# Optimization experiments

Measured on AMD Instinct MI355X. Metric: run time of the kernel, lower is better.

Reference implementation:

```python
import jax, jax.numpy as jnp
import numpy as np

NEG_INF = jnp.float32(-2**32 + 1)  # matches the module's padding constant


def setup_inputs() -> dict:
    key = jax.random.key(0)
    ks = jax.random.split(key, 20)
    T, N, E, R = 4, 20000, 320000, 2
    Din, Dh, H = 64, 64, 4
    s = 0.1  # xavier-ish scale
    inp = {
        "x": jax.random.normal(ks[0], (T, N, Din), jnp.float32),
        "edge_index": jax.random.randint(ks[1], (T, R, 2, E), 0, N, jnp.int32),
        "W_src": jax.random.normal(ks[2], (R, Din, H * Dh), jnp.float32) * s,
        "W_dst": jax.random.normal(ks[3], (R, Din, H * Dh), jnp.float32) * s,
        "att_src": jax.random.normal(ks[4], (R, H, Dh), jnp.float32) * s,
        "att_dst": jax.random.normal(ks[5], (R, H, Dh), jnp.float32) * s,
        "ra_W1": jax.random.normal(ks[6], (Dh, 4 * Dh), jnp.float32) * s,
        "ra_b1": jnp.zeros((4 * Dh,), jnp.float32),
        "ra_W2": jax.random.normal(ks[7], (4 * Dh, 1), jnp.float32) * s,
        "lstm_Wih": jax.random.normal(ks[8], (4 * Dh, Dh), jnp.float32) * s,
        "lstm_Whh": jax.random.normal(ks[9], (4 * Dh, Dh), jnp.float32) * s,
        "lstm_bih": jnp.zeros((4 * Dh,), jnp.float32),
        "lstm_bhh": jnp.zeros((4 * Dh,), jnp.float32),
        "pos_emb": jax.random.normal(ks[10], (T, Dh), jnp.float32) * s,
        "Wq": jax.random.normal(ks[11], (Dh, Dh), jnp.float32) * s,
        "Wk": jax.random.normal(ks[12], (Dh, Dh), jnp.float32) * s,
        "Wv": jax.random.normal(ks[13], (Dh, Dh), jnp.float32) * s,
    }
    return inp


def _gat(xt, ei, Ws, Wd, a_s, a_d, N, H, C):
    # PyG GATConv, concat=False, bias=False, eval mode (no dropout)
    src, dst = ei[0], ei[1]
    hs = (xt @ Ws).reshape(N, H, C)
    hd = (xt @ Wd).reshape(N, H, C)
    als = (hs * a_s[None]).sum(-1)          # [N,H]
    ald = (hd * a_d[None]).sum(-1)          # [N,H]
    e = jax.nn.leaky_relu(als[src] + ald[dst], 0.2)   # [E,H]
    m = jax.ops.segment_max(e, dst, num_segments=N)   # [N,H]
    p = jnp.exp(e - m[dst])
    denom = jax.ops.segment_sum(p, dst, num_segments=N)
    alpha = p / (denom[dst] + 1e-16)
    out = jax.ops.segment_sum(hs[src] * alpha[:, :, None], dst, num_segments=N)  # [N,H,C]
    return out.mean(1)                      # concat=False -> mean over heads


def reference(x, edge_index, W_src, W_dst, att_src, att_dst,
              ra_W1, ra_b1, ra_W2,
              lstm_Wih, lstm_Whh, lstm_bih, lstm_bhh,
              pos_emb, Wq, Wk, Wv):
    T, N, _ = x.shape
    R, H, C = att_src.shape   # C == n_hid (per-head GAT channels)

    # ---- intra-relation aggregation: GATConv per etype, vmapped over timeframes
    intra = []
    for r in range(R):
        f = jax.vmap(lambda xt, ei, r=r: _gat(xt, ei, W_src[r], W_dst[r],
                                              att_src[r], att_dst[r], N, H, C))
        intra.append(f(x, edge_index[:, r]))      # [T,N,C]
    h = jnp.stack(intra, axis=2)                  # [T,N,R,C]

    # ---- inter-relation aggregation (RelationAgg), batched over timeframes
    s = jnp.tanh(h @ ra_W1 + ra_b1) @ ra_W2       # [T,N,R,1]
    beta = jax.nn.softmax(s.mean(1), axis=1)      # mean over nodes, softmax over R -> [T,R,1]
    inter = (beta[:, None] * h).sum(2)            # [T,N,C]

    # ---- LSTM over time (batch = nodes)
    def step(carry, xt):
        hh, cc = carry
        g = xt @ lstm_Wih.T + hh @ lstm_Whh.T + lstm_bih + lstm_bhh
        i, f_, gg, o = jnp.split(g, 4, axis=-1)   # torch gate order i,f,g,o
        cc = jax.nn.sigmoid(f_) * cc + jax.nn.sigmoid(i) * jnp.tanh(gg)
        hh = jax.nn.sigmoid(o) * jnp.tanh(cc)
        return (hh, cc), hh
    z = jnp.zeros((N, C), x.dtype)
    _, hs_seq = jax.lax.scan(step, (z, z), inter)  # [T,N,C]
    feats = hs_seq.transpose(1, 0, 2)              # [N,T,C]

    # ---- temporal multi-head attention with causal mask, eval mode
    Ch = C // H
    ti = feats + pos_emb[None]                     # positions are just arange(T)
    qh = (ti @ Wq).reshape(N, T, H, Ch)
    kh = (ti @ Wk).reshape(N, T, H, Ch)
    vh = (ti @ Wv).reshape(N, T, H, Ch)
    scores = jnp.einsum('nqhc,nkhc->nhqk', qh, kh) / jnp.sqrt(jnp.float32(T))
    mask = jnp.tril(jnp.ones((T, T), bool))
    scores = jnp.where(mask[None, None], scores, NEG_INF)
    a = jax.nn.softmax(scores, axis=-1)
    out = jnp.einsum('nhqk,nkhc->nqhc', a, vh).reshape(N, T, C)
    return out  # output_features[ttype][ntype] == out[:, i, :]
```

## Files before the change

kernel.cpp:

```cpp
#include <hip/hip_runtime.h>
#include <hip/hip_bf16.h>

#define T_ 4
#define N_ 20000
#define E_ 320000
#define R_ 2
#define DIN 64
#define G_ 256
#define P_ 8
#define BPAD 16384
#define NB_ 32
#define EPB_ 10000
#define CHN_ 625

typedef unsigned short u16;
typedef __attribute__((ext_vector_type(8))) short bf16x8;
typedef __attribute__((ext_vector_type(2))) _Float16 h2;
typedef __attribute__((ext_vector_type(4))) float f32x4;

__device__ __forceinline__ float bf2f(u16 u) {
    unsigned int i = ((unsigned int)u) << 16; float f;
    __builtin_memcpy(&f, &i, 4); return f;
}
__device__ __forceinline__ u16 f2bf(float f) {
    unsigned int i; __builtin_memcpy(&i, &f, 4);
    unsigned int r = i + 0x7fffu + ((i >> 16) & 1u);
    return (u16)(r >> 16);
}
__device__ __forceinline__ u16 f2h(float f) {
    union { _Float16 h; u16 u; } c; c.h = (_Float16)f; return c.u;
}
__device__ __forceinline__ float sigm(float x) { return 1.f / (1.f + __expf(-x)); }
__device__ __forceinline__ float ftanh(float x) { return 1.f - 2.f / (__expf(2.f * x) + 1.f); }
__device__ __forceinline__ float rdlanef(float v, int l) {
    int i; __builtin_memcpy(&i, &v, 4);
    int r = __builtin_amdgcn_readlane(i, l);
    float f; __builtin_memcpy(&f, &r, 4); return f;
}
__device__ __forceinline__ float fdot2(h2 a, h2 b, float c) {
#if __has_builtin(__builtin_amdgcn_fdot2)
    return __builtin_amdgcn_fdot2(a, b, c, false);
#else
    float r;
    asm("v_dot2_f32_f16 %0, %1, %2, %3" : "=v"(r) : "v"(a), "v"(b), "v"(c));
    return r;
#endif
}
__device__ __forceinline__ unsigned cvtpk_bf16(float lo, float hi) {
    unsigned r;
    asm("v_cvt_pk_bf16_f32 %0, %1, %2" : "=v"(r) : "v"(lo), "v"(hi));
    return r;
}

__device__ __forceinline__ void gemm_direct(
    const u16* __restrict__ A, const u16* __restrict__ Bpad,
    int M, int Astride, int kchunks, int m0, f32x4* acc)
{
    const int tid = threadIdx.x;
    const int lane = tid & 63, wv = tid >> 6;
    const int col = lane & 15, quad = lane >> 4;
    #pragma unroll
    for (int cf = 0; cf < 16; ++cf) { acc[cf][0]=0.f; acc[cf][1]=0.f; acc[cf][2]=0.f; acc[cf][3]=0.f; }

    int row = m0 + wv * 16 + col;
    int row_c = (row < M) ? row : (M - 1);

    for (int kc = 0; kc < kchunks; ++kc) {
        #pragma unroll
        for (int ks = 0; ks < 2; ++ks) {
            bf16x8 a = *(const bf16x8*)(A + (size_t)row_c * Astride + kc * 64 + ks * 32 + quad * 8);
            const u16* bb = Bpad + kc * BPAD + ks * 32 + quad * 8;
            #pragma unroll
            for (int cf = 0; cf < 16; ++cf) {
                bf16x8 b = *(const bf16x8*)(bb + (cf * 16 + col) * 64);
                acc[cf] = __builtin_amdgcn_mfma_f32_16x16x32_bf16(a, b, acc[cf], 0, 0, 0);
            }
        }
    }
}

__global__ __launch_bounds__(256) void k_fold(
    const float* __restrict__ x, const float* __restrict__ wdall,
    float* __restrict__ als_all, float* __restrict__ ald_all, u16* __restrict__ x_h)
{
    __shared__ float wds[1024];
    {
        int tid = threadIdx.x;
        *(float4*)(wds + tid * 4) = *(const float4*)(wdall + tid * 4);
    }
    __syncthreads();

    int t = blockIdx.y;
    int idx = blockIdx.x * 256 + threadIdx.x;
    if (idx >= N_ * 4) return;
    int n = idx >> 2, q = idx & 3;
    const float* xr = x + ((size_t)t * N_ + n) * 64 + q * 16;
    float4 xv[4];
    #pragma unroll
    for (int i = 0; i < 4; ++i) xv[i] = *(const float4*)(xr + i * 4);

    {
        union { u16 h[16]; ushort4 s4[4]; } cv;
        #pragma unroll
        for (int i = 0; i < 4; ++i) {
            cv.h[i*4+0] = f2h(xv[i].x); cv.h[i*4+1] = f2h(xv[i].y);
            cv.h[i*4+2] = f2h(xv[i].z); cv.h[i*4+3] = f2h(xv[i].w);
        }
        u16* xo = x_h + ((size_t)t * N_ + n) * 64 + q * 16;
        #pragma unroll
        for (int i = 0; i < 4; ++i) *(ushort4*)(xo + i * 4) = cv.s4[i];
    }

    float s[16];
    #pragma unroll
    for (int i = 0; i < 16; ++i) s[i] = 0.f;
    #pragma unroll
    for (int i = 0; i < 4; ++i) {
        float xe[4] = {xv[i].x, xv[i].y, xv[i].z, xv[i].w};
        #pragma unroll
        for (int e = 0; e < 4; ++e) {
            int k = q * 16 + i * 4 + e;
            float xk = xe[e];
            #pragma unroll
            for (int tb = 0; tb < 4; ++tb) {
                float4 w = *(const float4*)(wds + tb * 256 + k * 4);
                s[tb*4+0] += xk * w.x; s[tb*4+1] += xk * w.y;
                s[tb*4+2] += xk * w.z; s[tb*4+3] += xk * w.w;
            }
        }
    }
    #pragma unroll
    for (int i = 0; i < 16; ++i) {
        s[i] += __shfl_xor(s[i], 1);
        s[i] += __shfl_xor(s[i], 2);
    }
    if (q == 0) {
        *(float4*)(als_all + ((size_t)(t*2+0) * N_ + n) * 4) = make_float4(s[0], s[1], s[2], s[3]);
        *(float4*)(als_all + ((size_t)(t*2+1) * N_ + n) * 4) = make_float4(s[4], s[5], s[6], s[7]);
        *(float4*)(ald_all + ((size_t)(t*2+0) * N_ + n) * 4) = make_float4(s[8], s[9], s[10], s[11]);
        *(float4*)(ald_all + ((size_t)(t*2+1) * N_ + n) * 4) = make_float4(s[12], s[13], s[14], s[15]);
    }
}

__global__ void k_prep(const float* __restrict__ Wdst, const float* __restrict__ att_dst,
                       const float* __restrict__ Wih, const float* __restrict__ Whh,
                       const float* __restrict__ bih, const float* __restrict__ bhh,
                       const float* __restrict__ Wsrc, const float* __restrict__ att_src,
                       const float* __restrict__ raW1,
                       const float* __restrict__ Wq, const float* __restrict__ Wk,
                       const float* __restrict__ Wv,
                       float* __restrict__ wdall, float* __restrict__ biasv,
                       u16* __restrict__ raW1_pad, u16* __restrict__ Wc_pad,
                       u16* __restrict__ qkv_pad, u16* __restrict__ postB_pad,
                       float* __restrict__ sspart)
{
    int tid = threadIdx.x, bid = blockIdx.x;
    if (bid == 0) {
        for (int i = tid; i < 1024; i += 256) sspart[i] = 0.f;
        int k = tid >> 2, h = tid & 3;
        for (int r = 0; r < 2; ++r) {
            float ss = 0.f, sd = 0.f;
            for (int c = 0; c < 64; ++c) {
                ss += Wsrc[((size_t)r * 64 + k) * 256 + h * 64 + c] * att_src[r * 256 + h * 64 + c];
                sd += Wdst[((size_t)r * 64 + k) * 256 + h * 64 + c] * att_dst[r * 256 + h * 64 + c];
            }
            wdall[r * 256 + k * 4 + h] = ss;
            wdall[512 + r * 256 + k * 4 + h] = sd;
        }
        biasv[tid] = bih[tid] + bhh[tid];
    }
    for (int i = bid * 256 + tid; i < BPAD; i += gridDim.x * 256) {
        int n = i >> 6, kk = i & 63;
        raW1_pad[i] = f2bf(raW1[kk * 256 + n]);
    }
    for (int i = bid * 256 + tid; i < 2 * BPAD; i += gridDim.x * 256) {
        int kc = i >> 14, q = i & (BPAD - 1), n = q >> 6, kk = q & 63;
        const float* W = kc ? Whh : Wih;
        Wc_pad[i] = f2bf(W[n * 64 + kk]);
    }
    for (int i = bid * 256 + tid; i < 192 * 64; i += gridDim.x * 256) {
        int g = i >> 6, kk = i & 63;
        int j = g >> 6, c = g & 63;
        const float* W = (j == 0) ? Wq : (j == 1) ? Wk : Wv;
        qkv_pad[i] = f2bf(W[kk * 64 + c]);
    }
    for (int i = bid * 256 + tid; i < 2 * 4 * 4096; i += gridDim.x * 256) {
        int r = i >> 14, q = i & 16383, kc = q >> 12, qq = q & 4095;
        int c = qq >> 6, kk = qq & 63;
        int d = kc * 16 + (kk >> 2), h = kk & 3;
        postB_pad[i] = f2bf(Wsrc[(size_t)r * 16384 + d * 256 + h * 64 + c]);
    }
}

__global__ __launch_bounds__(256) void k_hist(const int* __restrict__ ei,
                                              u16* __restrict__ rank, u16* __restrict__ partial)
{
    __shared__ unsigned int hist[N_ / 2];
    int b = blockIdx.x, p = blockIdx.y, tid = threadIdx.x;
    for (int i = tid; i < N_ / 2; i += 256) hist[i] = 0u;
    __syncthreads();
    const int* dsts = ei + ((size_t)p * 2 + 1) * E_ + b * EPB_;
    u16* rk = rank + (size_t)p * E_ + b * EPB_;
    for (int e = tid; e < EPB_; e += 256) {
        int dst = dsts[e];
        unsigned sh = (unsigned)(dst & 1) * 16u;
        unsigned old = atomicAdd(&hist[dst >> 1], 1u << sh);
        rk[e] = (u16)((old >> sh) & 0xffffu);
    }
    __syncthreads();
    u16* part = partial + ((size_t)p * NB_ + b) * N_;
    for (int n = tid; n < N_; n += 256) {
        unsigned hv = hist[n >> 1];
        part[n] = (u16)((hv >> ((unsigned)(n & 1) * 16u)) & 0xffffu);
    }
}

__global__ __launch_bounds__(256) void k_scan1(u16* __restrict__ partial,
                                               int* __restrict__ offsets, int* __restrict__ chunktot)
{
    int p = blockIdx.y, ch = blockIdx.x;
    int tid = threadIdx.x, lane = tid & 63, wid = tid >> 6;
    __shared__ int wtot[4];
    u16* part = partial + (size_t)p * NB_ * N_;
    int* ofs = offsets + (size_t)p * (N_ + 1);
    int n0 = ch * CHN_;
    int carry = 0;
    for (int rnd = 0; rnd < 3; ++rnd) {
        int i = rnd * 256 + tid;
        int n = n0 + i;
        int v = 0;
        if (i < CHN_) {
            int run = 0;
            #pragma unroll 8
            for (int b = 0; b < NB_; ++b) {
                int pv = part[b * N_ + n];
                part[b * N_ + n] = (u16)run;
                run += pv;
            }
            v = run;
        }
        int incl = v;
        for (int d = 1; d < 64; d <<= 1) { int u = __shfl_up(incl, d); if (lane >= d) incl += u; }
        if (lane == 63) wtot[wid] = incl;
        __syncthreads();
        if (tid < 4) {
            int iv = wtot[tid];
            for (int d = 1; d < 4; d <<= 1) { int u = __shfl_up(iv, d); if (tid >= d) iv += u; }
            wtot[tid] = iv;
        }
        __syncthreads();
        int woff = (wid > 0) ? wtot[wid - 1] : 0;
        int tot = wtot[3];
        int excl = carry + woff + incl - v;
        if (i < CHN_) ofs[n] = excl;
        carry += tot;
        __syncthreads();
    }
    if (tid == 0) chunktot[p * NB_ + ch] = carry;
}

__global__ void k_scan3(int* __restrict__ offsets, const int* __restrict__ chunktot) {
    __shared__ int cb[NB_];
    int p = blockIdx.y;
    int tid = threadIdx.x;
    if (tid < 64) {
        int v = (tid < NB_) ? chunktot[p * NB_ + tid] : 0;
        #pragma unroll
        for (int d = 1; d < NB_; d <<= 1) { int u = __shfl_up(v, d); if (tid >= d) v += u; }
        if (tid < NB_) cb[tid] = v;
    }
    __syncthreads();
    int n = blockIdx.x * 256 + tid;
    if (n < N_) {
        int c = n / CHN_;
        int base = (c > 0) ? cb[c - 1] : 0;
        offsets[(size_t)p * (N_ + 1) + n] += base;
    }
    if (n == 0)
        offsets[(size_t)p * (N_ + 1) + N_] = E_;
}

__global__ void k_scatter(const int* __restrict__ ei, const int* __restrict__ offsets,
                          const u16* __restrict__ rank, const u16* __restrict__ partial,
                          u16* __restrict__ csr) {
    int bid = blockIdx.x;
    int p = bid & 7;
    int e = (bid >> 3) * 256 + threadIdx.x;
    int src = ei[((size_t)p * 2 + 0) * E_ + e];
    int dst = ei[((size_t)p * 2 + 1) * E_ + e];
    int b = e / EPB_;
    int pos = offsets[p * (N_ + 1) + dst]
            + (int)partial[((size_t)p * NB_ + b) * N_ + dst]
            + (int)rank[(size_t)p * E_ + e];
    csr[(size_t)p * E_ + pos] = (u16)src;
}

__global__ __launch_bounds__(256) void k_agg(
    const int* __restrict__ offsets, const u16* __restrict__ csr,
    const float* __restrict__ als_all, const float* __restrict__ ald_all,
    const u16* __restrict__ x_h, u16* __restrict__ xagg4)
{
    __shared__ __align__(16) u16 ptab[4][4][64];
    const int bid = blockIdx.x;
    const int p = bid & 7;
    const int t = p >> 1;
    const int* off   = offsets + (size_t)p * (N_ + 1);
    const u16* srcs  = csr + (size_t)p * E_;
    const float* als = als_all + (size_t)p * N_ * 4;
    const float* ald = ald_all + (size_t)p * N_ * 4;
    const u16* xb    = x_h + (size_t)t * N_ * 64;

    const int tid = threadIdx.x, lane = tid & 63, wv = tid >> 6;
    const int g = lane >> 4, el = lane & 15;
    const int n0 = (bid >> 3) * 16 + wv * 4;
    const int ng = n0 + g;
    const int o0 = off[ng], o1 = off[ng + 1];
    const int deg = o1 - o0;
    const float4 aldv = *(const float4*)(ald + (size_t)ng * 4);
    u16* pt = &ptab[wv][0][0];
    const int pw = g * 64 + (el >> 1) * 8 + (el & 1);

    int sdeg[4];
    #pragma unroll
    for (int q = 0; q < 4; ++q) sdeg[q] = __builtin_amdgcn_readlane(deg, q * 16);
    int mdeg = max(max(sdeg[0], sdeg[1]), max(sdeg[2], sdeg[3]));
    int nrounds = (mdeg + 15) >> 4;

    float acc[4][4];
    #pragma unroll
    for (int q = 0; q < 4; ++q)
        #pragma unroll
        for (int h = 0; h < 4; ++h) acc[q][h] = 0.f;
    float d0 = 0.f, d1 = 0.f, d2 = 0.f, d3 = 0.f;

    for (int rr = 0; rr < nrounds; ++rr) {
        int e = rr * 16 + el;
        int sv = 0;
        float p0 = 0.f, p1 = 0.f, p2 = 0.f, p3 = 0.f;
        if (e < deg) {
            sv = (int)srcs[o0 + e];
            float4 av = *(const float4*)(als + (size_t)sv * 4);
            float e0 = av.x + aldv.x, e1 = av.y + aldv.y;
            float e2 = av.z + aldv.z, e3 = av.w + aldv.w;
            e0 = fmaxf(e0, 0.2f * e0); e1 = fmaxf(e1, 0.2f * e1);
            e2 = fmaxf(e2, 0.2f * e2); e3 = fmaxf(e3, 0.2f * e3);
            p0 = __expf(e0); p1 = __expf(e1); p2 = __expf(e2); p3 = __expf(e3);
        }
        d0 += p0; d1 += p1; d2 += p2; d3 += p3;
        pt[pw + 0] = f2h(p0); pt[pw + 2] = f2h(p1);
        pt[pw + 4] = f2h(p2); pt[pw + 6] = f2h(p3);
        #pragma unroll
        for (int q = 0; q < 4; ++q) {
            int rem = sdeg[q] - rr * 16;
            if (rem > 0) {
                const u16* ptq = pt + q * 64;
                unsigned xl0[8], xl1[8];
                #pragma unroll
                for (int pr = 0; pr < 8; ++pr) {
                    if (pr * 2 < rem) {
                        int s0i = __builtin_amdgcn_readlane(sv, q * 16 + pr * 2);
                        int s1i = __builtin_amdgcn_readlane(sv, q * 16 + pr * 2 + 1);
                        xl0[pr] = xb[((size_t)(unsigned)s0i << 6) + lane];
                        xl1[pr] = xb[((size_t)(unsigned)s1i << 6) + lane];
                    }
                }
                #pragma unroll
                for (int pr = 0; pr < 8; ++pr) {
                    if (pr * 2 < rem) {
                        unsigned xp = xl0[pr] | (xl1[pr] << 16);
                        uint4 ppv = *(const uint4*)(ptq + pr * 8);
                        h2 xv, q0, q1, q2, q3;
                        __builtin_memcpy(&xv, &xp, 4);
                        __builtin_memcpy(&q0, &ppv.x, 4);
                        __builtin_memcpy(&q1, &ppv.y, 4);
                        __builtin_memcpy(&q2, &ppv.z, 4);
                        __builtin_memcpy(&q3, &ppv.w, 4);
                        acc[q][0] = fdot2(xv, q0, acc[q][0]);
                        acc[q][1] = fdot2(xv, q1, acc[q][1]);
                        acc[q][2] = fdot2(xv, q2, acc[q][2]);
                        acc[q][3] = fdot2(xv, q3, acc[q][3]);
                    }
                }
            }
        }
    }
    d0 += __shfl_xor(d0, 1); d0 += __shfl_xor(d0, 2);
    d0 += __shfl_xor(d0, 4); d0 += __shfl_xor(d0, 8);
    d1 += __shfl_xor(d1, 1); d1 += __shfl_xor(d1, 2);
    d1 += __shfl_xor(d1, 4); d1 += __shfl_xor(d1, 8);
    d2 += __shfl_xor(d2, 1); d2 += __shfl_xor(d2, 2);
    d2 += __shfl_xor(d2, 4); d2 += __shfl_xor(d2, 8);
    d3 += __shfl_xor(d3, 1); d3 += __shfl_xor(d3, 2);
    d3 += __shfl_xor(d3, 4); d3 += __shfl_xor(d3, 8);
    float inv0 = 0.25f / (d0 + 1e-16f);
    float inv1 = 0.25f / (d1 + 1e-16f);
    float inv2 = 0.25f / (d2 + 1e-16f);
    float inv3 = 0.25f / (d3 + 1e-16f);
    #pragma unroll
    for (int q = 0; q < 4; ++q) {
        float s0 = rdlanef(inv0, q * 16);
        float s1 = rdlanef(inv1, q * 16);
        float s2 = rdlanef(inv2, q * 16);
        float s3 = rdlanef(inv3, q * 16);
        unsigned w01 = cvtpk_bf16(acc[q][0] * s0, acc[q][1] * s1);
        unsigned w23 = cvtpk_bf16(acc[q][2] * s2, acc[q][3] * s3);
        *(uint2*)(xagg4 + ((size_t)p * N_ + n0 + q) * 256 + lane * 4) = make_uint2(w01, w23);
    }
}

__global__ __launch_bounds__(256) void k_post(
    const u16* __restrict__ xagg4, const u16* __restrict__ postB_pad,
    u16* __restrict__ intra)
{
    const int t = blockIdx.z, r = blockIdx.y;
    const u16* A = xagg4 + ((size_t)(t * 2 + r)) * N_ * 256;
    const u16* Bp = postB_pad + (size_t)r * 4 * 4096;
    const int tid = threadIdx.x, lane = tid & 63, wv = tid >> 6;
    const int col = lane & 15, quad = lane >> 4;
    int m0 = blockIdx.x * 64;
    int row = m0 + wv * 16 + col;
    int row_c = (row < N_) ? row : (N_ - 1);

    f32x4 acc[4];
    #pragma unroll
    for (int cf = 0; cf < 4; ++cf) { acc[cf][0]=0.f; acc[cf][1]=0.f; acc[cf][2]=0.f; acc[cf][3]=0.f; }
    #pragma unroll
    for (int kc = 0; kc < 4; ++kc) {
        #pragma unroll
        for (int ks = 0; ks < 2; ++ks) {
            bf16x8 a = *(const bf16x8*)(A + (size_t)row_c * 256 + kc * 64 + ks * 32 + quad * 8);
            const u16* bb = Bp + kc * 4096 + ks * 32 + quad * 8;
            #pragma unroll
            for (int cf = 0; cf < 4; ++cf) {
                bf16x8 b = *(const bf16x8*)(bb + (cf * 16 + col) * 64);
                acc[cf] = __builtin_amdgcn_mfma_f32_16x16x32_bf16(a, b, acc[cf], 0, 0, 0);
            }
        }
    }
    int rowbase = m0 + wv * 16 + quad * 4;
    #pragma unroll
    for (int cf = 0; cf < 4; ++cf) {
        int c = cf * 16 + col;
        #pragma unroll
        for (int reg = 0; reg < 4; ++reg) {
            int rr = rowbase + reg;
            if (rr < N_)
                intra[(((size_t)t * N_ + rr) * 2 + r) * 64 + c] = f2bf(acc[cf][reg]);
        }
    }
}

__global__ __launch_bounds__(256) void k_relagg(
    const u16* __restrict__ A, const u16* __restrict__ W1pad, const float* __restrict__ b1,
    const float* __restrict__ W2, float* __restrict__ sspart)
{
    int m0 = blockIdx.x * 64;
    f32x4 acc[16];
    gemm_direct(A, W1pad, T_ * N_ * R_, 64, 1, m0, acc);

    const int tid = threadIdx.x, lane = tid & 63, wv = tid >> 6;
    const int col = lane & 15;
    float sp[4] = {0.f, 0.f, 0.f, 0.f};
    #pragma unroll
    for (int cf = 0; cf < 16; ++cf) {
        int gcol = cf * 16 + col;
        float bb = b1[gcol];
        float ww = W2[gcol];
        #pragma unroll
        for (int reg = 0; reg < 4; ++reg)
            sp[reg] += ftanh(acc[cf][reg] + bb) * ww;
    }
    #pragma unroll
    for (int reg = 0; reg < 4; ++reg) {
        float v = sp[reg];
        v += __shfl_xor(v, 1); v += __shfl_xor(v, 2);
        v += __shfl_xor(v, 4); v += __shfl_xor(v, 8);
        sp[reg] = v;
    }
    float se = sp[0] + sp[2];
    float so = sp[1] + sp[3];
    se += __shfl_xor(se, 16); se += __shfl_xor(se, 32);
    so += __shfl_xor(so, 16); so += __shfl_xor(so, 32);
    __shared__ float red[8];
    if (lane == 0) { red[wv * 2] = se; red[wv * 2 + 1] = so; }
    __syncthreads();
    if (tid == 0) {
        float s0 = red[0] + red[2] + red[4] + red[6];
        float s1 = red[1] + red[3] + red[5] + red[7];
        int t = m0 / (N_ * R_);
        float* line = sspart + (blockIdx.x & 63) * 16;
        atomicAdd(&line[t * 2 + 0], s0);
        atomicAdd(&line[t * 2 + 1], s1);
    }
}

__global__ __launch_bounds__(256) void k_lstm(
    const u16* __restrict__ intra, const float* __restrict__ sspart,
    const u16* __restrict__ Wc_pad, const float* __restrict__ biasv,
    u16* __restrict__ feats)
{
    __shared__ __align__(16) u16 wtab[512][64];
    __shared__ __align__(16) u16 hl[64][72];
    __shared__ float betas_s[8];
    const int tid = threadIdx.x, lane = tid & 63, wv = tid >> 6;
    const int col = lane & 15, quad = lane >> 4;
    int m0 = blockIdx.x * 64;
    int row = m0 + wv * 16 + col;
    int row_c = (row < N_) ? row : (N_ - 1);
    int rowbase = m0 + wv * 16 + quad * 4;

    bf16x8 pi[4][4];
    #pragma unroll
    for (int t = 0; t < 4; ++t) {
        const u16* ib = intra + ((size_t)t * N_ + row_c) * 128;
        #pragma unroll
        for (int k = 0; k < 4; ++k)
            pi[t][k] = *(const bf16x8*)(ib + k * 32 + quad * 8);
    }

    {
        const uint4* src = (const uint4*)Wc_pad;
        #pragma unroll
        for (int it = 0; it < 16; ++it) {
            int u = it * 256 + tid;
            int r = u >> 3, s = u & 7;
            uint4 v = src[u];
            *(uint4*)((char*)&wtab[0][0] + (size_t)r * 128 + ((s ^ (r & 7)) * 16)) = v;
        }
    }
    if (tid < 64) {
        float a8[8];
        #pragma unroll
        for (int s = 0; s < 8; ++s) a8[s] = sspart[tid * 16 + s];
        #pragma unroll
        for (int s = 0; s < 8; ++s) {
            float v = a8[s];
            v += __shfl_xor(v, 1); v += __shfl_xor(v, 2);
            v += __shfl_xor(v, 4); v += __shfl_xor(v, 8);
            v += __shfl_xor(v, 16); v += __shfl_xor(v, 32);
            a8[s] = v;
        }
        if (tid < 4) {
            float s0 = a8[tid * 2] * (1.f / N_), s1 = a8[tid * 2 + 1] * (1.f / N_);
            float mx = fmaxf(s0, s1);
            float e0 = __expf(s0 - mx), e1 = __expf(s1 - mx);
            float inv = 1.f / (e0 + e1);
            betas_s[tid * 2] = e0 * inv; betas_s[tid * 2 + 1] = e1 * inv;
        }
    }
    __syncthreads();
    float betas[8];
    #pragma unroll
    for (int i = 0; i < 8; ++i) betas[i] = betas_s[i];

    float cc[4][4];
    #pragma unroll
    for (int j = 0; j < 4; ++j)
        #pragma unroll
        for (int reg = 0; reg < 4; ++reg) cc[j][reg] = 0.f;

    const int c7 = col & 7;
    #pragma unroll
    for (int t = 0; t < 4; ++t) {
        float b0 = betas[t * 2], b1 = betas[t * 2 + 1];

        f32x4 acc[16];
        #pragma unroll
        for (int cf = 0; cf < 16; ++cf) { acc[cf][0]=0.f; acc[cf][1]=0.f; acc[cf][2]=0.f; acc[cf][3]=0.f; }

        #pragma unroll
        for (int ks = 0; ks < 2; ++ks) {
            bf16x8 i0 = pi[t][ks];
            bf16x8 i1 = pi[t][2 + ks];
            union { u16 h[8]; bf16x8 v; } cv;
            #pragma unroll
            for (int j = 0; j < 8; ++j)
                cv.h[j] = f2bf(b0 * bf2f((u16)i0[j]) + b1 * bf2f((u16)i1[j]));
            #pragma unroll
            for (int cf = 0; cf < 16; ++cf) {
                bf16x8 b = *(const bf16x8*)((const char*)&wtab[0][0]
                    + (size_t)(cf * 16 + col) * 128 + (((ks * 4 + quad) ^ c7) * 16));
                acc[cf] = __builtin_amdgcn_mfma_f32_16x16x32_bf16(cv.v, b, acc[cf], 0, 0, 0);
            }
        }
        if (t > 0) {
            #pragma unroll
            for (int ks = 0; ks < 2; ++ks) {
                bf16x8 a = *(const bf16x8*)&hl[wv * 16 + col][ks * 32 + quad * 8];
                #pragma unroll
                for (int cf = 0; cf < 16; ++cf) {
                    bf16x8 b = *(const bf16x8*)((const char*)&wtab[0][0]
                        + (size_t)(256 + cf * 16 + col) * 128 + (((ks * 4 + quad) ^ c7) * 16));
                    acc[cf] = __builtin_amdgcn_mfma_f32_16x16x32_bf16(a, b, acc[cf], 0, 0, 0);
                }
            }
        }

        #pragma unroll
        for (int j = 0; j < 4; ++j) {
            int c = j * 16 + col;
            float bi = biasv[c], bf_ = biasv[64 + c], bg = biasv[128 + c], bo = biasv[192 + c];
            #pragma unroll
            for (int reg = 0; reg < 4; ++reg) {
                float gi = acc[j][reg] + bi;
                float gf = acc[j + 4][reg] + bf_;
                float gg = acc[j + 8][reg] + bg;
                float go = acc[j + 12][reg] + bo;
                float c2 = sigm(gf) * cc[j][reg] + sigm(gi) * ftanh(gg);
                float hh = sigm(go) * ftanh(c2);
                cc[j][reg] = c2;
                u16 hb = f2bf(hh);
                hl[wv * 16 + quad * 4 + reg][c] = hb;
                int rr = rowbase + reg;
                if (rr < N_)
                    feats[(size_t)rr * 256 + t * 64 + c] = hb;
            }
        }
    }
}

__global__ __launch_bounds__(256) void k_attn(
    const u16* __restrict__ feats, const float* __restrict__ pos_emb,
    const u16* __restrict__ qkv_pad, float* __restrict__ out)
{
    __shared__ float qkv_s[64 * 200];
    const int tid = threadIdx.x, lane = tid & 63, wv = tid >> 6;
    const int col = lane & 15, quad = lane >> 4;
    int m0 = blockIdx.x * 64;
    int row = m0 + wv * 16 + col;
    int trow = row & 3;

    f32x4 acc[12];
    #pragma unroll
    for (int cf = 0; cf < 12; ++cf) { acc[cf][0]=0.f; acc[cf][1]=0.f; acc[cf][2]=0.f; acc[cf][3]=0.f; }
    #pragma unroll
    for (int ks = 0; ks < 2; ++ks) {
        int coff = ks * 32 + quad * 8;
        bf16x8 fv = *(const bf16x8*)(feats + (size_t)row * 64 + coff);
        float4 p0 = *(const float4*)(pos_emb + trow * 64 + coff);
        float4 p1 = *(const float4*)(pos_emb + trow * 64 + coff + 4);
        union { u16 h[8]; bf16x8 v; } cv;
        cv.h[0] = f2bf(bf2f((u16)fv[0]) + p0.x); cv.h[1] = f2bf(bf2f((u16)fv[1]) + p0.y);
        cv.h[2] = f2bf(bf2f((u16)fv[2]) + p0.z); cv.h[3] = f2bf(bf2f((u16)fv[3]) + p0.w);
        cv.h[4] = f2bf(bf2f((u16)fv[4]) + p1.x); cv.h[5] = f2bf(bf2f((u16)fv[5]) + p1.y);
        cv.h[6] = f2bf(bf2f((u16)fv[6]) + p1.z); cv.h[7] = f2bf(bf2f((u16)fv[7]) + p1.w);
        bf16x8 a = cv.v;
        const u16* bb = qkv_pad + ks * 32 + quad * 8;
        #pragma unroll
        for (int cf = 0; cf < 12; ++cf) {
            bf16x8 b = *(const bf16x8*)(bb + (cf * 16 + col) * 64);
            acc[cf] = __builtin_amdgcn_mfma_f32_16x16x32_bf16(a, b, acc[cf], 0, 0, 0);
        }
    }
    #pragma unroll
    for (int cf = 0; cf < 12; ++cf) {
        int g = cf * 16 + col;
        #pragma unroll
        for (int reg = 0; reg < 4; ++reg) {
            int rl = wv * 16 + quad * 4 + reg;
            qkv_s[rl * 200 + g] = acc[cf][reg];
        }
    }
    __syncthreads();

    int nl = wv * 4 + (lane >> 4);
    int sub = lane & 15;
    int h = sub >> 2, tq = sub & 3;
    const float* qrow = qkv_s + (nl * 4 + tq) * 200 + h * 16;

    float s[4];
    #pragma unroll
    for (int tk = 0; tk < 4; ++tk) {
        const float* krow = qkv_s + (nl * 4 + tk) * 200 + 64 + h * 16;
        float d = 0.f;
        #pragma unroll
        for (int j = 0; j < 16; ++j) d += qrow[j] * krow[j];
        s[tk] = (tk > tq) ? -4294967295.0f : d * 0.5f;
    }
    float mx = fmaxf(fmaxf(s[0], s[1]), fmaxf(s[2], s[3]));
    float a0 = __expf(s[0]-mx), a1 = __expf(s[1]-mx), a2 = __expf(s[2]-mx), a3 = __expf(s[3]-mx);
    float inv = 1.f / (a0 + a1 + a2 + a3);
    a0 *= inv; a1 *= inv; a2 *= inv; a3 *= inv;

    int n = blockIdx.x * 16 + nl;
    const float* v0 = qkv_s + (nl * 4 + 0) * 200 + 128 + h * 16;
    const float* v1 = v0 + 200, *v2 = v0 + 400, *v3 = v0 + 600;
    #pragma unroll
    for (int cc4 = 0; cc4 < 4; ++cc4) {
        float4 o;
        o.x = a0*v0[cc4*4+0] + a1*v1[cc4*4+0] + a2*v2[cc4*4+0] + a3*v3[cc4*4+0];
        o.y = a0*v0[cc4*4+1] + a1*v1[cc4*4+1] + a2*v2[cc4*4+1] + a3*v3[cc4*4+1];
        o.z = a0*v0[cc4*4+2] + a1*v1[cc4*4+2] + a2*v2[cc4*4+2] + a3*v3[cc4*4+2];
        o.w = a0*v0[cc4*4+3] + a1*v1[cc4*4+3] + a2*v2[cc4*4+3] + a3*v3[cc4*4+3];
        *(float4*)(out + (size_t)n * 256 + tq * 64 + h * 16 + cc4 * 4) = o;
    }
}

extern "C" void kernel_launch(void* const* d_in, const int* in_sizes, int n_in,
                              void* d_out, int out_size, void* d_ws, size_t ws_size,
                              hipStream_t stream) {
    const float* x     = (const float*)d_in[0];
    const int* ei      = (const int*)d_in[1];
    const float* Wsrc  = (const float*)d_in[2];
    const float* Wdst  = (const float*)d_in[3];
    const float* att_src = (const float*)d_in[4];
    const float* att_dst = (const float*)d_in[5];
    const float* raW1  = (const float*)d_in[6];
    const float* rab1  = (const float*)d_in[7];
    const float* raW2  = (const float*)d_in[8];
    const float* Wih   = (const float*)d_in[9];
    const float* Whh   = (const float*)d_in[10];
    const float* bih   = (const float*)d_in[11];
    const float* bhh   = (const float*)d_in[12];
    const float* pos   = (const float*)d_in[13];
    const float* Wq    = (const float*)d_in[14];
    const float* Wk    = (const float*)d_in[15];
    const float* Wv    = (const float*)d_in[16];
    float* out = (float*)d_out;

    char* w = (char*)d_ws;
    size_t off = 0;
    auto alloc = [&](size_t bytes) -> char* {
        char* pp = w + off; off += (bytes + 255) & ~(size_t)255; return pp;
    };
    u16*   intra     = (u16*)  alloc((size_t)T_ * N_ * R_ * 64 * 2);
    u16*   x_h       = (u16*)  alloc((size_t)T_ * N_ * 64 * 2);
    float* sspart    = (float*)alloc(1024 * 4);
    float* wdall     = (float*)alloc(1024 * 4);
    float* biasv     = (float*)alloc(256 * 4);
    u16*   raW1_pad  = (u16*)  alloc(BPAD * 2);
    u16*   Wc_pad    = (u16*)  alloc(2 * BPAD * 2);
    u16*   qkv_pad   = (u16*)  alloc(192 * 64 * 2);
    u16*   postB_pad = (u16*)  alloc(2 * 4 * 4096 * 2);
    int*   chunktot  = (int*)  alloc(P_ * NB_ * 4);
    char*  ubase   = alloc(0);
    size_t uoff = 0;
    auto ualloc = [&](size_t bytes) -> char* {
        char* pp = ubase + uoff; uoff += (bytes + 255) & ~(size_t)255; return pp;
    };
    int*   offsets = (int*)  ualloc((size_t)P_ * (N_ + 1) * 4);
    u16*   csr     = (u16*)  ualloc((size_t)P_ * E_ * 2);
    float* als_all = (float*)ualloc((size_t)P_ * N_ * 4 * 4);
    float* ald_all = (float*)ualloc((size_t)P_ * N_ * 4 * 4);
    u16*   partial = (u16*)  ualloc((size_t)P_ * NB_ * N_ * 2);
    u16*   xagg4   = (u16*)  ualloc((size_t)P_ * N_ * 256 * 2);
    u16*   rank    = (u16*)  xagg4;
    u16*   feats   = (u16*)  ubase;
    (void)ws_size; (void)in_sizes; (void)n_in; (void)out_size;

    k_prep<<<72, 256, 0, stream>>>(Wdst, att_dst, Wih, Whh, bih, bhh, Wsrc, att_src, raW1,
                                   Wq, Wk, Wv, wdall, biasv, raW1_pad, Wc_pad, qkv_pad,
                                   postB_pad, sspart);
    k_hist<<<dim3(NB_, 8), 256, 0, stream>>>(ei, rank, partial);
    k_scan1<<<dim3(NB_, 8), 256, 0, stream>>>(partial, offsets, chunktot);
    k_scan3<<<dim3(79, 8), 256, 0, stream>>>(offsets, chunktot);
    k_scatter<<<10000, 256, 0, stream>>>(ei, offsets, rank, partial, csr);
    k_fold<<<dim3(313, 4), 256, 0, stream>>>(x, wdall, als_all, ald_all, x_h);
    k_agg<<<10000, 256, 0, stream>>>(offsets, csr, als_all, ald_all, x_h, xagg4);
    k_post<<<dim3(313, 2, 4), 256, 0, stream>>>(xagg4, postB_pad, intra);
    k_relagg<<<2500, 256, 0, stream>>>(intra, raW1_pad, rab1, raW2, sspart);
    k_lstm<<<313, 256, 0, stream>>>(intra, sspart, Wc_pad, biasv, feats);
    k_attn<<<1250, 256, 0, stream>>>(feats, pos, qkv_pad, out);
}
```

Baseline: 419.6 us.

## Fuse post-aggregation projection GEMM into k_agg via swizzled shared tile

The separate k_post kernel is removed. k_agg now stages its 16x256 bf16 per-head aggregates in an XOR-swizzled shared buffer and runs the projection with MFMA directly, writing intra. This avoids a 41 MB xagg4 round trip through global memory and one kernel launch. A second change adds a fast path for full 16-edge rounds that skips the per-pair bound checks. The cost is extra LDS, a __syncthreads, and a small MFMA tail in every block.

After: 397.9 us. 1.05x faster.

```diff
diff --git a/kernel.cpp b/kernel.cpp
--- a/kernel.cpp
+++ b/kernel.cpp
@@ -298,12 +298,14 @@
 __global__ __launch_bounds__(256) void k_agg(
     const int* __restrict__ offsets, const u16* __restrict__ csr,
     const float* __restrict__ als_all, const float* __restrict__ ald_all,
-    const u16* __restrict__ x_h, u16* __restrict__ xagg4)
+    const u16* __restrict__ x_h, const u16* __restrict__ postB_pad,
+    u16* __restrict__ intra)
 {
     __shared__ __align__(16) u16 ptab[4][4][64];
+    __shared__ __align__(16) u16 xs[16 * 256];
     const int bid = blockIdx.x;
     const int p = bid & 7;
-    const int t = p >> 1;
+    const int t = p >> 1, rel = p & 1;
     const int* off   = offsets + (size_t)p * (N_ + 1);
     const u16* srcs  = csr + (size_t)p * E_;
     const float* als = als_all + (size_t)p * N_ * 4;
@@ -312,7 +314,8 @@
 
     const int tid = threadIdx.x, lane = tid & 63, wv = tid >> 6;
     const int g = lane >> 4, el = lane & 15;
-    const int n0 = (bid >> 3) * 16 + wv * 4;
+    const int nb0 = (bid >> 3) * 16;
+    const int n0 = nb0 + wv * 4;
     const int ng = n0 + g;
     const int o0 = off[ng], o1 = off[ng + 1];
     const int deg = o1 - o0;
@@ -352,7 +355,32 @@
         #pragma unroll
         for (int q = 0; q < 4; ++q) {
             int rem = sdeg[q] - rr * 16;
-            if (rem > 0) {
+            if (rem >= 16) {
+                const u16* ptq = pt + q * 64;
+                unsigned xl0[8], xl1[8];
+                #pragma unroll
+                for (int pr = 0; pr < 8; ++pr) {
+                    int s0i = __builtin_amdgcn_readlane(sv, q * 16 + pr * 2);
+                    int s1i = __builtin_amdgcn_readlane(sv, q * 16 + pr * 2 + 1);
+                    xl0[pr] = xb[((size_t)(unsigned)s0i << 6) + lane];
+                    xl1[pr] = xb[((size_t)(unsigned)s1i << 6) + lane];
+                }
+                #pragma unroll
+                for (int pr = 0; pr < 8; ++pr) {
+                    unsigned xp = xl0[pr] | (xl1[pr] << 16);
+                    uint4 ppv = *(const uint4*)(ptq + pr * 8);
+                    h2 xv, q0, q1, q2, q3;
+                    __builtin_memcpy(&xv, &xp, 4);
+                    __builtin_memcpy(&q0, &ppv.x, 4);
+                    __builtin_memcpy(&q1, &ppv.y, 4);
+                    __builtin_memcpy(&q2, &ppv.z, 4);
+                    __builtin_memcpy(&q3, &ppv.w, 4);
+                    acc[q][0] = fdot2(xv, q0, acc[q][0]);
+                    acc[q][1] = fdot2(xv, q1, acc[q][1]);
+                    acc[q][2] = fdot2(xv, q2, acc[q][2]);
+                    acc[q][3] = fdot2(xv, q3, acc[q][3]);
+                }
+            } else if (rem > 0) {
                 const u16* ptq = pt + q * 64;
                 unsigned xl0[8], xl1[8];
                 #pragma unroll
@@ -404,48 +432,31 @@
         float s3 = rdlanef(inv3, q * 16);
         unsigned w01 = cvtpk_bf16(acc[q][0] * s0, acc[q][1] * s1);
         unsigned w23 = cvtpk_bf16(acc[q][2] * s2, acc[q][3] * s3);
-        *(uint2*)(xagg4 + ((size_t)p * N_ + n0 + q) * 256 + lane * 4) = make_uint2(w01, w23);
-    }
-}
-
-__global__ __launch_bounds__(256) void k_post(
-    const u16* __restrict__ xagg4, const u16* __restrict__ postB_pad,
-    u16* __restrict__ intra)
-{
-    const int t = blockIdx.z, r = blockIdx.y;
-    const u16* A = xagg4 + ((size_t)(t * 2 + r)) * N_ * 256;
-    const u16* Bp = postB_pad + (size_t)r * 4 * 4096;
-    const int tid = threadIdx.x, lane = tid & 63, wv = tid >> 6;
-    const int col = lane & 15, quad = lane >> 4;
-    int m0 = blockIdx.x * 64;
-    int row = m0 + wv * 16 + col;
-    int row_c = (row < N_) ? row : (N_ - 1);
-
-    f32x4 acc[4];
-    #pragma unroll
-    for (int cf = 0; cf < 4; ++cf) { acc[cf][0]=0.f; acc[cf][1]=0.f; acc[cf][2]=0.f; acc[cf][3]=0.f; }
-    #pragma unroll
-    for (int kc = 0; kc < 4; ++kc) {
-        #pragma unroll
-        for (int ks = 0; ks < 2; ++ks) {
-            bf16x8 a = *(const bf16x8*)(A + (size_t)row_c * 256 + kc * 64 + ks * 32 + quad * 8);
-            const u16* bb = Bp + kc * 4096 + ks * 32 + quad * 8;
+        int rowt = wv * 4 + q;
+        char* dst = (char*)xs + rowt * 512 + (((lane >> 1) ^ (rowt & 7)) * 16) + (lane & 1) * 8;
+        *(uint2*)dst = make_uint2(w01, w23);
+    }
+    __syncthreads();
+
+    {
+        const int col = lane & 15, quad = lane >> 4;
+        const u16* Bp = postB_pad + (size_t)rel * 4 * 4096;
+        f32x4 pacc;
+        pacc[0] = 0.f; pacc[1] = 0.f; pacc[2] = 0.f; pacc[3] = 0.f;
+        #pragma unroll
+        for (int kc = 0; kc < 4; ++kc) {
             #pragma unroll
-            for (int cf = 0; cf < 4; ++cf) {
-                bf16x8 b = *(const bf16x8*)(bb + (cf * 16 + col) * 64);
-                acc[cf] = __builtin_amdgcn_mfma_f32_16x16x32_bf16(a, b, acc[cf], 0, 0, 0);
-            }
-        }
-    }
-    int rowbase = m0 + wv * 16 + quad * 4;
-    #pragma unroll
-    for (int cf = 0; cf < 4; ++cf) {
-        int c = cf * 16 + col;
+            for (int ks = 0; ks < 2; ++ks) {
+                int slot = kc * 8 + ks * 4 + quad;
+                bf16x8 a = *(const bf16x8*)((const char*)xs + col * 512 + ((slot ^ (col & 7)) * 16));
+                bf16x8 b = *(const bf16x8*)(Bp + (size_t)kc * 4096 + (wv * 16 + col) * 64 + ks * 32 + quad * 8);
+                pacc = __builtin_amdgcn_mfma_f32_16x16x32_bf16(a, b, pacc, 0, 0, 0);
+            }
+        }
         #pragma unroll
         for (int reg = 0; reg < 4; ++reg) {
-            int rr = rowbase + reg;
-            if (rr < N_)
-                intra[(((size_t)t * N_ + rr) * 2 + r) * 64 + c] = f2bf(acc[cf][reg]);
+            int node = nb0 + quad * 4 + reg;
+            intra[(((size_t)t * N_ + node) * 2 + rel) * 64 + wv * 16 + col] = f2bf(pacc[reg]);
         }
     }
 }
@@ -743,8 +754,7 @@
     float* als_all = (float*)ualloc((size_t)P_ * N_ * 4 * 4);
     float* ald_all = (float*)ualloc((size_t)P_ * N_ * 4 * 4);
     u16*   partial = (u16*)  ualloc((size_t)P_ * NB_ * N_ * 2);
-    u16*   xagg4   = (u16*)  ualloc((size_t)P_ * N_ * 256 * 2);
-    u16*   rank    = (u16*)  xagg4;
+    u16*   rank    = (u16*)  ualloc((size_t)P_ * E_ * 2);
     u16*   feats   = (u16*)  ubase;
     (void)ws_size; (void)in_sizes; (void)n_in; (void)out_size;
 
@@ -756,8 +766,7 @@
     k_scan3<<<dim3(79, 8), 256, 0, stream>>>(offsets, chunktot);
     k_scatter<<<10000, 256, 0, stream>>>(ei, offsets, rank, partial, csr);
     k_fold<<<dim3(313, 4), 256, 0, stream>>>(x, wdall, als_all, ald_all, x_h);
-    k_agg<<<10000, 256, 0, stream>>>(offsets, csr, als_all, ald_all, x_h, xagg4);
-    k_post<<<dim3(313, 2, 4), 256, 0, stream>>>(xagg4, postB_pad, intra);
+    k_agg<<<10000, 256, 0, stream>>>(offsets, csr, als_all, ald_all, x_h, postB_pad, intra);
     k_relagg<<<2500, 256, 0, stream>>>(intra, raW1_pad, rab1, raW2, sspart);
     k_lstm<<<313, 256, 0, stream>>>(intra, sspart, Wc_pad, biasv, feats);
     k_attn<<<1250, 256, 0, stream>>>(feats, pos, qkv_pad, out);
```
